# Kernel optimization log

Hardware: AMD Instinct MI355X
Metric: run time of the kernel (lower is better)

## Reference

```python
import jax, jax.numpy as jnp
import numpy as np


def setup_inputs() -> dict:
    key = jax.random.key(0)
    k1, k2, k3 = jax.random.split(key, 3)
    B, T, N, D = 16, 12, 4096, 64
    M = 128  # memory_num
    return {
        "nodevec1": jax.random.normal(k1, (B, T, N, D), dtype=jnp.float32),
        "nodevec2": jax.random.normal(k2, (B, T, N, D), dtype=jnp.float32),
        "node_embeddings": jax.random.normal(k3, (M, 2 * D), dtype=jnp.float32),
        "topk": 32,
    }


def reference(nodevec1, nodevec2, node_embeddings, topk):
    B, T, N, D = nodevec1.shape
    M = node_embeddings.shape[0]
    # nodevec3: [B,T,N,2D] matches node_embeddings' 2*time_dim trailing dim
    nodevec3 = jnp.concatenate([nodevec1, nodevec2], axis=-1)
    # attention-like map over nodes: [B,T,M,N]
    logits = jnp.einsum('me,btne->btmn', node_embeddings, nodevec3)
    supports2 = jax.nn.softmax(logits, axis=-1)
    values, indices = jax.lax.top_k(supports2, topk)  # [B,T,M,K], sorted desc

    def gather(x):
        # gather K nodes per memory slot along the N axis
        idx = indices.reshape(B, T, M * topk, 1)  # [B,T,M*K,1]
        g = jnp.take_along_axis(x, idx, axis=2)   # [B,T,M*K,D]
        return g.reshape(B, T, M, topk, D)

    sel1 = gather(nodevec1)
    sel2 = gather(nodevec2)
    batch_indices = jnp.broadcast_to(jnp.arange(B).reshape(B, 1, 1, 1), (B, T, M, topk))
    time_indices = jnp.broadcast_to(jnp.arange(T).reshape(1, T, 1, 1), (B, T, M, topk))
    return (sel1, sel2, batch_indices, time_indices, indices)
```

## Files before the change

### kernel.cpp

```cpp
#include <hip/hip_runtime.h>
#include <stdint.h>

typedef unsigned long long u64;
typedef unsigned short u16;
typedef __attribute__((ext_vector_type(8))) short short8;
typedef __attribute__((ext_vector_type(4))) float f32x4;

#define NB   16
#define NT   12
#define BTc  192
#define NN   4096
#define DD   64
#define MM   128
#define TOPK 32
#define KTH  44
#define CAP  128

#define SEL1_OFF 0ULL
#define SEL2_OFF 50331648ULL
#define BIDX_OFF 100663296ULL
#define TIDX_OFF 101449728ULL
#define IDX_OFF  102236160ULL

__device__ __forceinline__ unsigned ord32(float f) {
    unsigned u = __float_as_uint(f);
    return (u & 0x80000000u) ? ~u : (u | 0x80000000u);
}
__device__ __forceinline__ u16 f2bf(float f) {
    unsigned u = __float_as_uint(f);
    unsigned r = u + 0x7FFFu + ((u >> 16) & 1u);
    return (u16)(r >> 16);
}
__device__ __forceinline__ float bf2f(short s) {
    return __uint_as_float(((unsigned)(u16)s) << 16);
}
__device__ __forceinline__ u64 pack4bf(float4 v) {
    return (u64)f2bf(v.x) | ((u64)f2bf(v.y) << 16) |
           ((u64)f2bf(v.z) << 32) | ((u64)f2bf(v.w) << 48);
}
__device__ __forceinline__ void lds_fence() {
    asm volatile("s_waitcnt lgkmcnt(0)" ::: "memory");
    __builtin_amdgcn_sched_barrier(0);
}
__device__ __forceinline__ float sort64f_desc(float v, int l) {
#pragma unroll
    for (int k = 2; k <= 64; k <<= 1) {
#pragma unroll
        for (int j = k >> 1; j >= 1; j >>= 1) {
            float o = __shfl_xor(v, j);
            bool takeMax = (((l & j) == 0) == ((l & k) == 0));
            v = takeMax ? fmaxf(v, o) : fminf(v, o);
        }
    }
    return v;
}
__device__ __forceinline__ u64 sort64_desc(u64 v, int l) {
#pragma unroll
    for (int k = 2; k <= 64; k <<= 1) {
#pragma unroll
        for (int j = k >> 1; j >= 1; j >>= 1) {
            u64 o = __shfl_xor(v, j);
            bool takeMax = (((l & j) == 0) == ((l & k) == 0));
            v = takeMax ? (v > o ? v : o) : (v < o ? v : o);
        }
    }
    return v;
}

__global__ __launch_bounds__(256) void k1_logits_bf16(const float* __restrict__ nv1,
                                                      const float* __restrict__ nv2,
                                                      const float* __restrict__ emb,
                                                      float* __restrict__ outBase) {
    u16* logitsB = (u16*)outBase;
    __shared__ u16 Als[128 * 128];
    __shared__ u16 Bls[128 * 128];

    const int tid = threadIdx.x;
    const int nt  = blockIdx.x;
    const int bt  = blockIdx.y;
    const int n0  = nt * 128;

#pragma unroll
    for (int it = 0; it < 16; ++it) {
        int f4  = it * 256 + tid;
        int row = f4 >> 5;
        int kq  = f4 & 31;
        float4 a = *(const float4*)(emb + row * 128 + kq * 4);
        int byte = row * 256 + ((kq * 8) ^ ((row & 7) << 4));
        *(u64*)((char*)Als + byte) = pack4bf(a);
    }
#pragma unroll
    for (int it = 0; it < 16; ++it) {
        int f4  = it * 256 + tid;
        int row = f4 >> 5;
        int kq  = f4 & 31;
        const float* src = (kq < 16)
            ? (nv1 + ((size_t)bt * NN + n0 + row) * DD + kq * 4)
            : (nv2 + ((size_t)bt * NN + n0 + row) * DD + (kq - 16) * 4);
        float4 bv = *(const float4*)src;
        int byte = row * 256 + ((kq * 8) ^ ((row & 7) << 4));
        *(u64*)((char*)Bls + byte) = pack4bf(bv);
    }
    __syncthreads();

    const int w  = tid >> 6;
    const int l  = tid & 63;
    const int mb = (w >> 1) * 64;
    const int nb = (w & 1) * 64;
    const int xr = (l & 7) << 4;

    f32x4 acc[4][4];
#pragma unroll
    for (int mi = 0; mi < 4; ++mi)
#pragma unroll
        for (int ni = 0; ni < 4; ++ni) acc[mi][ni] = {0.f, 0.f, 0.f, 0.f};

#pragma unroll
    for (int ks = 0; ks < 4; ++ks) {
        const int kb = (ks * 64 + (l >> 4) * 16) ^ xr;
        short8 a[4], b[4];
#pragma unroll
        for (int mi = 0; mi < 4; ++mi) {
            int row = mb + mi * 16 + (l & 15);
            a[mi] = *(const short8*)((const char*)Als + row * 256 + kb);
        }
#pragma unroll
        for (int ni = 0; ni < 4; ++ni) {
            int row = nb + ni * 16 + (l & 15);
            b[ni] = *(const short8*)((const char*)Bls + row * 256 + kb);
        }
#pragma unroll
        for (int mi = 0; mi < 4; ++mi)
#pragma unroll
            for (int ni = 0; ni < 4; ++ni)
                acc[mi][ni] = __builtin_amdgcn_mfma_f32_16x16x32_bf16(
                    a[mi], b[ni], acc[mi][ni], 0, 0, 0);
    }

    const size_t rbase = (size_t)bt * MM * NN;
#pragma unroll
    for (int mi = 0; mi < 4; ++mi)
#pragma unroll
        for (int ni = 0; ni < 4; ++ni) {
            int n = n0 + nb + ni * 16 + (l & 15);
#pragma unroll
            for (int r = 0; r < 4; ++r) {
                int m = mb + mi * 16 + (l >> 4) * 4 + r;
                logitsB[rbase + (size_t)m * NN + n] = f2bf(acc[mi][ni][r]);
            }
        }

    u16* sum_lo = (u16*)((char*)outBase + BIDX_OFF * 4);
    u16* sum_hi = (u16*)((char*)outBase + TIDX_OFF * 4);
#pragma unroll
    for (int mi = 0; mi < 4; ++mi)
#pragma unroll
        for (int pr = 0; pr < 2; ++pr)
#pragma unroll
            for (int r = 0; r < 4; ++r) {
                float v = fmaxf(bf2f((short)f2bf(acc[mi][pr * 2][r])),
                                bf2f((short)f2bf(acc[mi][pr * 2 + 1][r])));
#pragma unroll
                for (int mk = 1; mk < 16; mk <<= 1)
                    v = fmaxf(v, __shfl_xor(v, mk));
                if ((l & 15) == 0) {
                    int m   = mb + mi * 16 + (l >> 4) * 4 + r;
                    int g   = nt * 4 + (nb >> 5) + pr;
                    int rw  = bt * MM + m;
                    u16 hv  = f2bf(v);
                    if (g < 64) sum_lo[rw * 64 + g]        = hv;
                    else        sum_hi[rw * 64 + (g - 64)] = hv;
                }
            }
}

__global__ __launch_bounds__(256) void k2_fused(const u16* logitsB,
                                                const float* __restrict__ nv1,
                                                const float* __restrict__ nv2,
                                                const float* __restrict__ emb,
                                                float* out) {
    const int tid = threadIdx.x;
    const int l   = tid & 63;
    const int w   = tid >> 6;
    const int bid = (int)blockIdx.x;
    const int swz = (bid & 7) * 768 + (bid >> 3);
    const int row = swz * 4 + w;
    const int bt  = row >> 7;
    const int m   = row & 127;
    const u16* src = logitsB + (size_t)row * NN;

    __shared__ int   cand[4][CAP];
    __shared__ int   glist[4][128];
    __shared__ float embrow[4][128];

    embrow[w][l]      = emb[m * 128 + l];
    embrow[w][l + 64] = emb[m * 128 + 64 + l];

    const u16* sum_lo = (const u16*)((const char*)out + BIDX_OFF * 4) + row * 64;
    const u16* sum_hi = (const u16*)((const char*)out + TIDX_OFF * 4) + row * 64;
    const float gm0 = bf2f((short)sum_lo[l]);
    const float gm1 = bf2f((short)sum_hi[l]);

    const float A = sort64f_desc(gm0, l);
    const float B = sort64f_desc(gm1, l);
    const float INF = __builtin_inff();
    float av = __shfl(A, (l >= 1) ? l - 1 : 0);
    if (l < 1) av = INF;
    int jb = KTH - 1 - l;
    float bv = __shfl(B, (jb >= 0 && jb < 64) ? jb : 0);
    if (jb < 0) bv = INF;
    float mm = (l <= KTH) ? fminf(av, bv) : -INF;
#pragma unroll
    for (int mk = 1; mk < 64; mk <<= 1)
        mm = fmaxf(mm, __shfl_xor(mm, mk));
    const float T = mm;

    u64 m0 = __ballot(gm0 >= T);
    u64 m1 = __ballot(gm1 >= T);
    const u64 below = (1ull << l) - 1ull;
    const int n0q = (int)__popcll(m0);
    if (gm0 >= T) glist[w][__popcll(m0 & below)] = l;
    if (gm1 >= T) glist[w][n0q + (int)__popcll(m1 & below)] = 64 + l;
    const int ng = n0q + (int)__popcll(m1);
    lds_fence();

    int c = 0;
    const int rounds = (ng + 15) >> 4;
    for (int rd = 0; rd < rounds; ++rd) {
        int gi = rd * 16 + (l >> 2);
        bool act = gi < ng;
        int g = act ? glist[w][gi] : 0;
        short8 v8 = {0, 0, 0, 0, 0, 0, 0, 0};
        if (act) v8 = *(const short8*)(src + g * 32 + (l & 3) * 8);
        int nbase = g * 32 + (l & 3) * 8;
#pragma unroll
        for (int e = 0; e < 8; ++e) {
            bool p = act && (bf2f(v8[e]) >= T);
            u64 mask = __ballot(p);
            if (p) {
                int pos = c + (int)__popcll(mask & below);
                if (pos < CAP) cand[w][pos] = nbase + e;
            }
            c += (int)__popcll(mask);
        }
    }
    if (c > CAP) c = CAP;
    lds_fence();

    u64 kreg[2] = {0ull, 0ull};
    const int nch = (c + 63) >> 6;
    for (int s3 = 0; s3 < nch; ++s3) {
        int s = s3 * 64 + l;
        if (s < c) {
            int n = cand[w][s];
            const float4* c1 = (const float4*)(nv1 + ((size_t)bt * NN + n) * DD);
            const float4* c2 = (const float4*)(nv2 + ((size_t)bt * NN + n) * DD);
            float acc = 0.f;
#pragma unroll
            for (int q = 0; q < 16; ++q) {
                float4 x = c1[q];
                acc = fmaf(embrow[w][q * 4 + 0], x.x, acc);
                acc = fmaf(embrow[w][q * 4 + 1], x.y, acc);
                acc = fmaf(embrow[w][q * 4 + 2], x.z, acc);
                acc = fmaf(embrow[w][q * 4 + 3], x.w, acc);
            }
#pragma unroll
            for (int q = 0; q < 16; ++q) {
                float4 x = c2[q];
                acc = fmaf(embrow[w][64 + q * 4 + 0], x.x, acc);
                acc = fmaf(embrow[w][64 + q * 4 + 1], x.y, acc);
                acc = fmaf(embrow[w][64 + q * 4 + 2], x.z, acc);
                acc = fmaf(embrow[w][64 + q * 4 + 3], x.w, acc);
            }
            kreg[s3] = ((u64)ord32(acc) << 32) | (u64)(0xFFFFFFFFu - (unsigned)n);
        }
    }

    u64 top = sort64_desc(kreg[0], l);
    if (c > 64) {
        u64 Bk = sort64_desc(kreg[1], l);
        u64 rb = __shfl_xor(Bk, 63);
        u64 M = top > rb ? top : rb;
#pragma unroll
        for (int j = 32; j >= 1; j >>= 1) {
            u64 o = __shfl_xor(M, j);
            M = ((l & j) == 0) ? (M > o ? M : o) : (M < o ? M : o);
        }
        top = M;
    }

    const int b = bt / NT;
    const int t = bt - b * NT;
    const size_t obase = (size_t)row * TOPK;
    const unsigned mynode = 0xFFFFFFFFu - (unsigned)(top & 0xFFFFFFFFull);
    if (l < TOPK) {
        out[IDX_OFF  + obase + l] = (float)mynode;
        out[BIDX_OFF + obase + l] = (float)b;
        out[TIDX_OFF + obase + l] = (float)t;
    }

    int myn[8];
#pragma unroll
    for (int it = 0; it < 8; ++it) {
        int p = it * 4 + (l >> 4);
        u64 kk = __shfl(top, p);
        myn[it] = (int)(0xFFFFFFFFu - (unsigned)(kk & 0xFFFFFFFFull)) & (NN - 1);
    }
    const int j4 = (l & 15) * 4;
#pragma unroll
    for (int it = 0; it < 8; ++it) {
        int p = it * 4 + (l >> 4);
        const float4 s1 = *(const float4*)(nv1 + ((size_t)bt * NN + myn[it]) * DD + j4);
        const float4 s2 = *(const float4*)(nv2 + ((size_t)bt * NN + myn[it]) * DD + j4);
        size_t o = (obase + p) * DD + j4;
        *(float4*)(out + SEL1_OFF + o) = s1;
        *(float4*)(out + SEL2_OFF + o) = s2;
    }
}

extern "C" void kernel_launch(void* const* d_in, const int* in_sizes, int n_in,
                              void* d_out, int out_size, void* d_ws, size_t ws_size,
                              hipStream_t stream) {
    const float* nv1 = (const float*)d_in[0];
    const float* nv2 = (const float*)d_in[1];
    const float* emb = (const float*)d_in[2];
    float* out = (float*)d_out;

    dim3 g1(32, BTc);
    k1_logits_bf16<<<g1, 256, 0, stream>>>(nv1, nv2, emb, out);
    k2_fused<<<24576 / 4, 256, 0, stream>>>((const u16*)d_out, nv1, nv2, emb, out);
}
```

Baseline: 447.0 us.

## Coalesce group-max scratch writes via LDS and split index-fill into separate kernel

The per-group max values in k1 are staged through shared memory and written as 64-bit coalesced stores into a transposed slab, replacing scattered 2-byte global stores. k2 now runs two rows per 128-thread block and reads its group maxima with a strided pattern from the new layout. The batch/time index fills move to a separate third kernel so they no longer overwrite the scratch slab while k2 still reads it. This trades an extra launch and strided reads in k2 for coalesced writes in k1 and removes the write/read conflict on the shared scratch region.

```diff
diff --git a/kernel.cpp b/kernel.cpp
--- a/kernel.cpp
+++ b/kernel.cpp
@@ -74,6 +74,7 @@
     u16* logitsB = (u16*)outBase;
     __shared__ u16 Als[128 * 128];
     __shared__ u16 Bls[128 * 128];
+    __shared__ u16 sumS[4 * 128];
 
     const int tid = threadIdx.x;
     const int nt  = blockIdx.x;
@@ -150,8 +151,6 @@
             }
         }
 
-    u16* sum_lo = (u16*)((char*)outBase + BIDX_OFF * 4);
-    u16* sum_hi = (u16*)((char*)outBase + TIDX_OFF * 4);
 #pragma unroll
     for (int mi = 0; mi < 4; ++mi)
 #pragma unroll
@@ -164,17 +163,21 @@
                 for (int mk = 1; mk < 16; mk <<= 1)
                     v = fmaxf(v, __shfl_xor(v, mk));
                 if ((l & 15) == 0) {
-                    int m   = mb + mi * 16 + (l >> 4) * 4 + r;
-                    int g   = nt * 4 + (nb >> 5) + pr;
-                    int rw  = bt * MM + m;
-                    u16 hv  = f2bf(v);
-                    if (g < 64) sum_lo[rw * 64 + g]        = hv;
-                    else        sum_hi[rw * 64 + (g - 64)] = hv;
+                    int m  = mb + mi * 16 + (l >> 4) * 4 + r;
+                    int gl = (nb >> 5) + pr;
+                    sumS[gl * 128 + m] = f2bf(v);
                 }
             }
-}
-
-__global__ __launch_bounds__(256) void k2_fused(const u16* logitsB,
+    __syncthreads();
+    if (tid < 128) {
+        u64 v = ((const u64*)sumS)[tid];
+        int gl = tid >> 5;
+        u64* slab64 = (u64*)((char*)outBase + BIDX_OFF * 4);
+        slab64[(size_t)bt * 4096 + (nt * 4 + gl) * 32 + (tid & 31)] = v;
+    }
+}
+
+__global__ __launch_bounds__(128) void k2_fused(const u16* logitsB,
                                                 const float* __restrict__ nv1,
                                                 const float* __restrict__ nv2,
                                                 const float* __restrict__ emb,
@@ -183,23 +186,22 @@
     const int l   = tid & 63;
     const int w   = tid >> 6;
     const int bid = (int)blockIdx.x;
-    const int swz = (bid & 7) * 768 + (bid >> 3);
-    const int row = swz * 4 + w;
+    const int swz = (bid & 7) * 1536 + (bid >> 3);
+    const int row = swz * 2 + w;
     const int bt  = row >> 7;
     const int m   = row & 127;
     const u16* src = logitsB + (size_t)row * NN;
 
-    __shared__ int   cand[4][CAP];
-    __shared__ int   glist[4][128];
-    __shared__ float embrow[4][128];
+    __shared__ int   cand[2][CAP];
+    __shared__ int   glist[2][128];
+    __shared__ float embrow[2][128];
+
+    const u16* slab = (const u16*)((const char*)out + BIDX_OFF * 4) + (size_t)bt * 16384;
+    const float gm0 = bf2f((short)slab[l * 128 + m]);
+    const float gm1 = bf2f((short)slab[(64 + l) * 128 + m]);
 
     embrow[w][l]      = emb[m * 128 + l];
     embrow[w][l + 64] = emb[m * 128 + 64 + l];
-
-    const u16* sum_lo = (const u16*)((const char*)out + BIDX_OFF * 4) + row * 64;
-    const u16* sum_hi = (const u16*)((const char*)out + TIDX_OFF * 4) + row * 64;
-    const float gm0 = bf2f((short)sum_lo[l]);
-    const float gm1 = bf2f((short)sum_hi[l]);
 
     const float A = sort64f_desc(gm0, l);
     const float B = sort64f_desc(gm1, l);
@@ -289,15 +291,9 @@
         top = M;
     }
 
-    const int b = bt / NT;
-    const int t = bt - b * NT;
     const size_t obase = (size_t)row * TOPK;
     const unsigned mynode = 0xFFFFFFFFu - (unsigned)(top & 0xFFFFFFFFull);
-    if (l < TOPK) {
-        out[IDX_OFF  + obase + l] = (float)mynode;
-        out[BIDX_OFF + obase + l] = (float)b;
-        out[TIDX_OFF + obase + l] = (float)t;
-    }
+    if (l < TOPK) out[IDX_OFF + obase + l] = (float)mynode;
 
     int myn[8];
 #pragma unroll
@@ -318,6 +314,13 @@
     }
 }
 
+__global__ __launch_bounds__(256) void k3_fill(float* out) {
+    int i   = blockIdx.x * 256 + threadIdx.x;
+    int bt  = i >> 12;
+    out[BIDX_OFF + i] = (float)(bt / NT);
+    out[TIDX_OFF + i] = (float)(bt - (bt / NT) * NT);
+}
+
 extern "C" void kernel_launch(void* const* d_in, const int* in_sizes, int n_in,
                               void* d_out, int out_size, void* d_ws, size_t ws_size,
                               hipStream_t stream) {
@@ -328,5 +331,6 @@
 
     dim3 g1(32, BTc);
     k1_logits_bf16<<<g1, 256, 0, stream>>>(nv1, nv2, emb, out);
-    k2_fused<<<24576 / 4, 256, 0, stream>>>((const u16*)d_out, nv1, nv2, emb, out);
-}
+    k2_fused<<<12288, 128, 0, stream>>>((const u16*)d_out, nv1, nv2, emb, out);
+    k3_fill<<<786432 / 256, 256, 0, stream>>>(out);
+}
```

Result: slower. 460.5 us (+3.0%).
